# Optimization experiments

Hardware: AMD Instinct MI355X
Metric: run time of the kernel (lower is better)

## Reference

```python
import jax, jax.numpy as jnp
import numpy as np

N = 100000        # nodes
E = 1600000       # edges (avg degree 16)
H = 128           # hidden dim
LAYERS = 3
RESIDUAL = 1.0


def setup_inputs() -> dict:
    key = jax.random.key(0)
    ks = jax.random.split(key, 7)
    x = jax.random.normal(ks[0], (N, H), dtype=jnp.float32)
    src = jax.random.randint(ks[1], (E,), 0, N, dtype=jnp.int32)
    dst = jax.random.randint(ks[2], (E,), 0, N, dtype=jnp.int32)
    s = 1.0 / np.sqrt(H)
    W1 = jax.random.normal(ks[3], (H, H), dtype=jnp.float32) * s
    b1 = jnp.zeros((H,), dtype=jnp.float32)
    W2 = jax.random.normal(ks[4], (H, H), dtype=jnp.float32) * s
    b2 = jnp.zeros((H,), dtype=jnp.float32)
    return {"x": x, "src": src, "dst": dst, "W1": W1, "b1": b1, "W2": W2, "b2": b2}


def _gcn_conv(h, src, dst, dinv, W, b):
    # PyG GCNConv: h' = D^{-1/2}(A+I)D^{-1/2} (h W) + b
    h = h @ W                                   # [N,H]
    norm = dinv[src] * dinv[dst]                # [E]
    msgs = h[src] * norm[:, None]               # [E,H] gather (memory-bound)
    agg = jax.ops.segment_sum(msgs, dst, num_segments=N)  # scatter-add
    agg = agg + h * (dinv * dinv)[:, None]      # self-loop contribution
    return agg + b


def reference(x, src, dst, W1, b1, W2, b2):
    # symmetric degree normalization with self-loops (deg over dst, + 1 for self-loop)
    deg = jax.ops.segment_sum(jnp.ones((E,), x.dtype), dst, num_segments=N) + 1.0
    dinv = jax.lax.rsqrt(deg)                   # [N]

    ori = x
    h = _gcn_conv(x, src, dst, dinv, W1, b1) + RESIDUAL * ori
    for _ in range(LAYERS - 1):
        h = jax.nn.relu(h)                      # dropout is identity in eval mode
        h = _gcn_conv(h, src, dst, dinv, W2, b2) + RESIDUAL * ori
    return h
```

## Files before the change

kernel.cpp:

```cpp
#include <hip/hip_runtime.h>

#define H 128
#define AP 136
#define BSH 9
#define BSZ 512
#define NBK 256

typedef __attribute__((ext_vector_type(8))) short short8;
typedef __attribute__((ext_vector_type(4))) float floatx4;
typedef __attribute__((ext_vector_type(2))) float f32x2;

__device__ inline unsigned short f2b(float f) {
  union { float f; unsigned u; } v; v.f = f;
  unsigned r = v.u + 0x7fffu + ((v.u >> 16) & 1u);
  return (unsigned short)(r >> 16);
}
__device__ inline float blo(unsigned u) { return __uint_as_float(u << 16); }
__device__ inline float bhi(unsigned u) { return __uint_as_float(u & 0xffff0000u); }
__device__ inline unsigned char f2f8(float f) {
  return (unsigned char)(__builtin_amdgcn_cvt_pk_fp8_f32(f, f, 0, false) & 0xff);
}
__device__ inline f32x2 fp8x2(unsigned u) {
#if __has_builtin(__builtin_amdgcn_cvt_pk_f32_fp8)
  return __builtin_amdgcn_cvt_pk_f32_fp8(u, false);
#else
  f32x2 r;
  r.x = __builtin_amdgcn_cvt_f32_fp8(u, 0);
  r.y = __builtin_amdgcn_cvt_f32_fp8(u, 1);
  return r;
#endif
}


__global__ __launch_bounds__(256) void k_bh(const int* __restrict__ dst,
                                            int* __restrict__ bhist,
                                            int E, int NB, int chunk) {
  __shared__ int hst[NBK];
  int tid = threadIdx.x;
  hst[tid] = 0;
  __syncthreads();
  int s = blockIdx.x * chunk;
  int eend = min(s + chunk, E);
  for (int e = s + tid; e < eend; e += 256)
    atomicAdd(&hst[dst[e] >> BSH], 1);
  __syncthreads();
  if (tid < NB) bhist[tid * NBK + blockIdx.x] = hst[tid];
}

__global__ __launch_bounds__(1024) void k_bscan(const int* __restrict__ bhist,
                                                int* __restrict__ boff2,
                                                int total) {
  __shared__ int ps[1024];
  int tid = threadIdx.x;
  int per = (total + 1023) >> 10;
  int s0 = min(tid * per, total), s1 = min(s0 + per, total);
  int sum = 0;
  for (int i = s0; i < s1; i++) sum += bhist[i];
  ps[tid] = sum;
  __syncthreads();
  for (int off = 1; off < 1024; off <<= 1) {
    int t = (tid >= off) ? ps[tid - off] : 0;
    __syncthreads();
    ps[tid] += t;
    __syncthreads();
  }
  int run = ps[tid] - sum;
  for (int i = s0; i < s1; i++) { int v = bhist[i]; boff2[i] = run; run += v; }
}

__global__ __launch_bounds__(256) void k_bscatter(const int* __restrict__ src,
                                                  const int* __restrict__ dst,
                                                  const int* __restrict__ boff2,
                                                  int* __restrict__ bed,
                                                  int E, int NB, int chunk) {
  __shared__ int pos[NBK];
  int tid = threadIdx.x;
  if (tid < NB) pos[tid] = boff2[tid * NBK + blockIdx.x];
  __syncthreads();
  int s = blockIdx.x * chunk;
  int eend = min(s + chunk, E);
  for (int e = s + tid; e < eend; e += 256) {
    int d = dst[e];
    int p = atomicAdd(&pos[d >> BSH], 1);
    bed[p] = (src[e] << BSH) | (d & (BSZ - 1));
  }
}

__global__ __launch_bounds__(512) void k_build(const int* __restrict__ bed,
                                               const int* __restrict__ boff2,
                                               int* __restrict__ roff,
                                               float* __restrict__ dinv,
                                               int* __restrict__ csr,
                                               int N, int E, int NB) {
  __shared__ int cnt[BSZ];
  __shared__ int pos[BSZ];
  __shared__ int ps[BSZ];
  int b = blockIdx.x, tid = threadIdx.x;
  int bs = boff2[b * NBK];
  int be = (b + 1 < NB) ? boff2[(b + 1) * NBK] : E;
  int n0 = b << BSH;
  cnt[tid] = 0;
  __syncthreads();
  for (int e = bs + tid; e < be; e += 512)
    atomicAdd(&cnt[bed[e] & (BSZ - 1)], 1);
  __syncthreads();
  int c = cnt[tid];
  ps[tid] = c;
  __syncthreads();
  for (int off = 1; off < 512; off <<= 1) {
    int t = (tid >= off) ? ps[tid - off] : 0;
    __syncthreads();
    ps[tid] += t;
    __syncthreads();
  }
  int base = bs + ps[tid] - c;
  pos[tid] = base;
  int node = n0 + tid;
  if (node < N) {
    roff[node] = base;
    dinv[node] = rsqrtf((float)c + 1.0f);
  }
  __syncthreads();
  for (int e = bs + tid; e < be; e += 512) {
    int v = bed[e];
    int p = atomicAdd(&pos[v & (BSZ - 1)], 1);
    csr[p] = v >> BSH;
  }
  if (b == 0 && tid == 0) roff[N] = E;
}

__global__ __launch_bounds__(256) void k_prep_w(const float* __restrict__ W1,
                                                const float* __restrict__ W2,
                                                unsigned short* __restrict__ Wt1,
                                                unsigned short* __restrict__ Wt2) {
  const float* W = blockIdx.x ? W2 : W1;
  unsigned short* Wt = blockIdx.x ? Wt2 : Wt1;
  int tid = threadIdx.x;
#pragma unroll
  for (int i = 0; i < 64; i++) {
    int idx = tid + 256 * i;
    int k = idx >> 7, n = idx & 127;
    Wt[n * 128 + k] = f2b(W[idx]);
  }
}

__global__ __launch_bounds__(256) void k_prep_xb(const float* __restrict__ x,
                                                 unsigned int* __restrict__ xb, int total) {
  int i = blockIdx.x * 256 + threadIdx.x;
  if (i < total) {
    float2 v = ((const float2*)x)[i];
    xb[i] = (unsigned)f2b(v.x) | ((unsigned)f2b(v.y) << 16);
  }
}

__global__ __launch_bounds__(256) void k_gemm(const unsigned int* __restrict__ in,
                                              const unsigned short* __restrict__ Wt,
                                              unsigned char* __restrict__ out,
                                              int n) {
  __shared__ short As[64 * AP];
  __shared__ short Bs[128 * AP];
  int tid = threadIdx.x;
  int wave = tid >> 6, lane = tid & 63;
  int quad = lane >> 4, l16 = lane & 15;
  int row0 = blockIdx.x * 64;

  const float4* in4 = (const float4*)in;
#pragma unroll
  for (int i = 0; i < 4; i++) {
    int idx = tid + 256 * i;
    int r = idx >> 4, c = idx & 15;
    int gr = row0 + r;
    float4 v = make_float4(0.f, 0.f, 0.f, 0.f);
    if (gr < n) v = in4[(size_t)gr * 16 + c];
    *(float4*)&As[r * AP + c * 8] = v;
  }
  const float4* Wt4 = (const float4*)Wt;
#pragma unroll
  for (int i = 0; i < 8; i++) {
    int idx = tid + 256 * i;
    int nr = idx >> 4, c = idx & 15;
    *(float4*)&Bs[nr * AP + c * 8] = Wt4[nr * 16 + c];
  }
  __syncthreads();

  floatx4 acc[4][2];
#pragma unroll
  for (int mt = 0; mt < 4; mt++)
#pragma unroll
    for (int nt = 0; nt < 2; nt++) acc[mt][nt] = (floatx4)(0.f);

#pragma unroll
  for (int ks = 0; ks < 4; ks++) {
    short8 a[4], b[2];
#pragma unroll
    for (int mt = 0; mt < 4; mt++)
      a[mt] = *(const short8*)&As[(mt * 16 + l16) * AP + ks * 32 + quad * 8];
#pragma unroll
    for (int nt = 0; nt < 2; nt++)
      b[nt] = *(const short8*)&Bs[(wave * 32 + nt * 16 + l16) * AP + ks * 32 + quad * 8];
#pragma unroll
    for (int mt = 0; mt < 4; mt++)
#pragma unroll
      for (int nt = 0; nt < 2; nt++)
        acc[mt][nt] = __builtin_amdgcn_mfma_f32_16x16x32_bf16(a[mt], b[nt], acc[mt][nt], 0, 0, 0);
  }

#pragma unroll
  for (int mt = 0; mt < 4; mt++) {
#pragma unroll
    for (int nt = 0; nt < 2; nt++) {
#pragma unroll
      for (int r = 0; r < 4; r++) {
        int gr = row0 + mt * 16 + quad * 4 + r;
        if (gr < n)
          out[(size_t)gr * H + wave * 32 + nt * 16 + l16] = f2f8(acc[mt][nt][r]);
      }
    }
  }
}

__global__ __launch_bounds__(256) void k_agg(const unsigned short* __restrict__ h,
                                             const int* __restrict__ csr,
                                             const int* __restrict__ roff,
                                             const float* __restrict__ dinv,
                                             const float* __restrict__ bias,
                                             const unsigned int* __restrict__ xb,
                                             float* __restrict__ out32,
                                             unsigned int* __restrict__ out16,
                                             int n, int write16) {
  int wave = threadIdx.x >> 6;
  int lane = threadIdx.x & 63;
  int node = blockIdx.x * 4 + wave;
  if (node >= n) return;

  float di = dinv[node];
  unsigned su = h[(size_t)node * 64 + lane];
  unsigned xu = xb[(size_t)node * 64 + lane];
  float2 bv = ((const float2*)bias)[lane];
  f32x2 sp = fp8x2(su);
  float acc0 = bv.x + blo(xu) + di * di * sp.x;
  float acc1 = bv.y + bhi(xu) + di * di * sp.y;

  int e0 = roff[node], e1 = roff[node + 1];
  int e = e0;
  for (; e + 16 <= e1; e += 16) {
    int eu = __builtin_amdgcn_readfirstlane(e);
    int idx[16];
#pragma unroll
    for (int k = 0; k < 16; k++) idx[k] = __builtin_amdgcn_readfirstlane(csr[eu + k]);
    unsigned u[16];
#pragma unroll
    for (int k = 0; k < 16; k++) u[k] = (h + ((size_t)idx[k] << 6))[lane];
    float cf[16];
#pragma unroll
    for (int k = 0; k < 16; k++) cf[k] = di * dinv[idx[k]];
#pragma unroll
    for (int k = 0; k < 16; k++) {
      f32x2 p = fp8x2(u[k]);
      acc0 += cf[k] * p.x;
      acc1 += cf[k] * p.y;
    }
  }
  for (; e + 4 <= e1; e += 4) {
    int eu = __builtin_amdgcn_readfirstlane(e);
    int idx[4];
#pragma unroll
    for (int k = 0; k < 4; k++) idx[k] = __builtin_amdgcn_readfirstlane(csr[eu + k]);
    unsigned u[4];
#pragma unroll
    for (int k = 0; k < 4; k++) u[k] = (h + ((size_t)idx[k] << 6))[lane];
    float cf[4];
#pragma unroll
    for (int k = 0; k < 4; k++) cf[k] = di * dinv[idx[k]];
#pragma unroll
    for (int k = 0; k < 4; k++) {
      f32x2 p = fp8x2(u[k]);
      acc0 += cf[k] * p.x;
      acc1 += cf[k] * p.y;
    }
  }
  for (; e < e1; e++) {
    int s = csr[e];
    float cf = di * dinv[s];
    unsigned u = h[(size_t)s * 64 + lane];
    f32x2 p = fp8x2(u);
    acc0 += cf * p.x;
    acc1 += cf * p.y;
  }
  if (write16) {
    out16[(size_t)node * 64 + lane] =
        (unsigned)f2b(fmaxf(acc0, 0.f)) | ((unsigned)f2b(fmaxf(acc1, 0.f)) << 16);
  } else {
    ((float2*)out32)[(size_t)node * 64 + lane] = make_float2(acc0, acc1);
  }
}

extern "C" void kernel_launch(void* const* d_in, const int* in_sizes, int n_in,
                              void* d_out, int out_size, void* d_ws, size_t ws_size,
                              hipStream_t stream) {
  const float* x = (const float*)d_in[0];
  const int* src = (const int*)d_in[1];
  const int* dst = (const int*)d_in[2];
  const float* W1 = (const float*)d_in[3];
  const float* b1 = (const float*)d_in[4];
  const float* W2 = (const float*)d_in[5];
  const float* b2 = (const float*)d_in[6];
  int N = in_sizes[0] / H;
  int E = in_sizes[1];
  float* out = (float*)d_out;

  char* p = (char*)d_ws;
  auto alloc = [&](size_t bytes) {
    char* q = p;
    p += (bytes + 255) & ~(size_t)255;
    return q;
  };
  int* roff = (int*)alloc((size_t)(N + 1) * 4);
  float* dinv = (float*)alloc((size_t)N * 4);
  int* csr = (int*)alloc((size_t)E * 4);
  unsigned int* xb = (unsigned int*)alloc((size_t)N * H * 2);
  unsigned char* htmp = (unsigned char*)alloc((size_t)N * H);
  unsigned int* fbuf = (unsigned int*)alloc((size_t)N * H * 2);
  unsigned short* Wt1 = (unsigned short*)alloc(128 * 128 * 2);
  unsigned short* Wt2 = (unsigned short*)alloc(128 * 128 * 2);
  int* bhist = (int*)alloc((size_t)NBK * NBK * 4);
  int* boff2 = (int*)alloc((size_t)NBK * NBK * 4);
  int* bed = (int*)alloc((size_t)E * 4);

  int NB = (N + BSZ - 1) >> BSH;
  int chunk = (E + NBK - 1) / NBK;

  k_bh<<<NBK, 256, 0, stream>>>(dst, bhist, E, NB, chunk);
  k_bscan<<<1, 1024, 0, stream>>>(bhist, boff2, NB * NBK);
  k_bscatter<<<NBK, 256, 0, stream>>>(src, dst, boff2, bed, E, NB, chunk);
  k_build<<<NB, 512, 0, stream>>>(bed, boff2, roff, dinv, csr, N, E, NB);

  k_prep_w<<<2, 256, 0, stream>>>(W1, W2, Wt1, Wt2);
  k_prep_xb<<<(N * (H / 2) + 255) / 256, 256, 0, stream>>>(x, xb, N * (H / 2));

  int gb = (N + 63) / 64;
  int ab = (N + 3) / 4;

  k_gemm<<<gb, 256, 0, stream>>>(xb, Wt1, htmp, N);
  k_agg<<<ab, 256, 0, stream>>>((const unsigned short*)htmp, csr, roff, dinv, b1, xb,
                                nullptr, fbuf, N, 1);
  k_gemm<<<gb, 256, 0, stream>>>(fbuf, Wt2, htmp, N);
  k_agg<<<ab, 256, 0, stream>>>((const unsigned short*)htmp, csr, roff, dinv, b2, xb,
                                nullptr, fbuf, N, 1);
  k_gemm<<<gb, 256, 0, stream>>>(fbuf, Wt2, htmp, N);
  k_agg<<<ab, 256, 0, stream>>>((const unsigned short*)htmp, csr, roff, dinv, b2, xb,
                                out, nullptr, N, 0);
}
```

Before: 458.6 us.

## Halve bucket-sort partition blocks, vectorize bucket scan, merge prep kernels

Cuts the bucket-sort partition count from 256 to 128 edge chunks and rewrites the offset scan to use one thread per bucket row with int4 loads and stores, replacing the strided 1024-thread scan. It also fuses the weight transpose and x-to-bf16 conversion into one launch, saving a kernel launch. Fewer chunks mean fewer histogram entries to scan, but k_bh and k_bscatter now run with less parallelism and more atomics per block.

```diff
diff --git a/kernel.cpp b/kernel.cpp
--- a/kernel.cpp
+++ b/kernel.cpp
@@ -4,7 +4,8 @@
 #define AP 136
 #define BSH 9
 #define BSZ 512
-#define NBK 256
+#define MAXB 256
+#define NBLK 128
 
 typedef __attribute__((ext_vector_type(8))) short short8;
 typedef __attribute__((ext_vector_type(4))) float floatx4;
@@ -35,7 +36,7 @@
 __global__ __launch_bounds__(256) void k_bh(const int* __restrict__ dst,
                                             int* __restrict__ bhist,
                                             int E, int NB, int chunk) {
-  __shared__ int hst[NBK];
+  __shared__ int hst[MAXB];
   int tid = threadIdx.x;
   hst[tid] = 0;
   __syncthreads();
@@ -44,28 +45,43 @@
   for (int e = s + tid; e < eend; e += 256)
     atomicAdd(&hst[dst[e] >> BSH], 1);
   __syncthreads();
-  if (tid < NB) bhist[tid * NBK + blockIdx.x] = hst[tid];
-}
-
-__global__ __launch_bounds__(1024) void k_bscan(const int* __restrict__ bhist,
-                                                int* __restrict__ boff2,
-                                                int total) {
-  __shared__ int ps[1024];
-  int tid = threadIdx.x;
-  int per = (total + 1023) >> 10;
-  int s0 = min(tid * per, total), s1 = min(s0 + per, total);
+  if (tid < NB) bhist[tid * NBLK + blockIdx.x] = hst[tid];
+}
+
+__global__ __launch_bounds__(256) void k_bscan(const int* __restrict__ bhist,
+                                               int* __restrict__ boff2, int NB) {
+  __shared__ int ps[256];
+  int tid = threadIdx.x;
+  int4 v[NBLK / 4];
   int sum = 0;
-  for (int i = s0; i < s1; i++) sum += bhist[i];
+  if (tid < NB) {
+    const int4* row = (const int4*)(bhist + tid * NBLK);
+#pragma unroll
+    for (int j = 0; j < NBLK / 4; j++) v[j] = row[j];
+#pragma unroll
+    for (int j = 0; j < NBLK / 4; j++) sum += v[j].x + v[j].y + v[j].z + v[j].w;
+  }
   ps[tid] = sum;
   __syncthreads();
-  for (int off = 1; off < 1024; off <<= 1) {
+  for (int off = 1; off < 256; off <<= 1) {
     int t = (tid >= off) ? ps[tid - off] : 0;
     __syncthreads();
     ps[tid] += t;
     __syncthreads();
   }
   int run = ps[tid] - sum;
-  for (int i = s0; i < s1; i++) { int v = bhist[i]; boff2[i] = run; run += v; }
+  if (tid < NB) {
+    int4* orow = (int4*)(boff2 + tid * NBLK);
+#pragma unroll
+    for (int j = 0; j < NBLK / 4; j++) {
+      int4 o;
+      o.x = run; run += v[j].x;
+      o.y = run; run += v[j].y;
+      o.z = run; run += v[j].z;
+      o.w = run; run += v[j].w;
+      orow[j] = o;
+    }
+  }
 }
 
 __global__ __launch_bounds__(256) void k_bscatter(const int* __restrict__ src,
@@ -73,9 +89,9 @@
                                                   const int* __restrict__ boff2,
                                                   int* __restrict__ bed,
                                                   int E, int NB, int chunk) {
-  __shared__ int pos[NBK];
-  int tid = threadIdx.x;
-  if (tid < NB) pos[tid] = boff2[tid * NBK + blockIdx.x];
+  __shared__ int pos[MAXB];
+  int tid = threadIdx.x;
+  if (tid < NB) pos[tid] = boff2[tid * NBLK + blockIdx.x];
   __syncthreads();
   int s = blockIdx.x * chunk;
   int eend = min(s + chunk, E);
@@ -96,8 +112,8 @@
   __shared__ int pos[BSZ];
   __shared__ int ps[BSZ];
   int b = blockIdx.x, tid = threadIdx.x;
-  int bs = boff2[b * NBK];
-  int be = (b + 1 < NB) ? boff2[(b + 1) * NBK] : E;
+  int bs = boff2[b * NBLK];
+  int be = (b + 1 < NB) ? boff2[(b + 1) * NBLK] : E;
   int n0 = b << BSH;
   cnt[tid] = 0;
   __syncthreads();
@@ -129,27 +145,28 @@
   if (b == 0 && tid == 0) roff[N] = E;
 }
 
-__global__ __launch_bounds__(256) void k_prep_w(const float* __restrict__ W1,
-                                                const float* __restrict__ W2,
-                                                unsigned short* __restrict__ Wt1,
-                                                unsigned short* __restrict__ Wt2) {
-  const float* W = blockIdx.x ? W2 : W1;
-  unsigned short* Wt = blockIdx.x ? Wt2 : Wt1;
-  int tid = threadIdx.x;
-#pragma unroll
-  for (int i = 0; i < 64; i++) {
-    int idx = tid + 256 * i;
-    int k = idx >> 7, n = idx & 127;
-    Wt[n * 128 + k] = f2b(W[idx]);
-  }
-}
-
-__global__ __launch_bounds__(256) void k_prep_xb(const float* __restrict__ x,
-                                                 unsigned int* __restrict__ xb, int total) {
-  int i = blockIdx.x * 256 + threadIdx.x;
-  if (i < total) {
-    float2 v = ((const float2*)x)[i];
-    xb[i] = (unsigned)f2b(v.x) | ((unsigned)f2b(v.y) << 16);
+__global__ __launch_bounds__(256) void k_prep(const float* __restrict__ W1,
+                                              const float* __restrict__ W2,
+                                              unsigned short* __restrict__ Wt1,
+                                              unsigned short* __restrict__ Wt2,
+                                              const float* __restrict__ x,
+                                              unsigned int* __restrict__ xb, int total) {
+  int tid = threadIdx.x;
+  if (blockIdx.x < 2) {
+    const float* W = blockIdx.x ? W2 : W1;
+    unsigned short* Wt = blockIdx.x ? Wt2 : Wt1;
+#pragma unroll
+    for (int i = 0; i < 64; i++) {
+      int idx = tid + 256 * i;
+      int k = idx >> 7, n = idx & 127;
+      Wt[n * 128 + k] = f2b(W[idx]);
+    }
+  } else {
+    int i = (blockIdx.x - 2) * 256 + tid;
+    if (i < total) {
+      float2 v = ((const float2*)x)[i];
+      xb[i] = (unsigned)f2b(v.x) | ((unsigned)f2b(v.y) << 16);
+    }
   }
 }
 
@@ -323,20 +340,20 @@
   unsigned int* fbuf = (unsigned int*)alloc((size_t)N * H * 2);
   unsigned short* Wt1 = (unsigned short*)alloc(128 * 128 * 2);
   unsigned short* Wt2 = (unsigned short*)alloc(128 * 128 * 2);
-  int* bhist = (int*)alloc((size_t)NBK * NBK * 4);
-  int* boff2 = (int*)alloc((size_t)NBK * NBK * 4);
+  int* bhist = (int*)alloc((size_t)MAXB * NBLK * 4);
+  int* boff2 = (int*)alloc((size_t)MAXB * NBLK * 4);
   int* bed = (int*)alloc((size_t)E * 4);
 
   int NB = (N + BSZ - 1) >> BSH;
-  int chunk = (E + NBK - 1) / NBK;
-
-  k_bh<<<NBK, 256, 0, stream>>>(dst, bhist, E, NB, chunk);
-  k_bscan<<<1, 1024, 0, stream>>>(bhist, boff2, NB * NBK);
-  k_bscatter<<<NBK, 256, 0, stream>>>(src, dst, boff2, bed, E, NB, chunk);
+  int chunk = (E + NBLK - 1) / NBLK;
+
+  k_bh<<<NBLK, 256, 0, stream>>>(dst, bhist, E, NB, chunk);
+  k_bscan<<<1, 256, 0, stream>>>(bhist, boff2, NB);
+  k_bscatter<<<NBLK, 256, 0, stream>>>(src, dst, boff2, bed, E, NB, chunk);
   k_build<<<NB, 512, 0, stream>>>(bed, boff2, roff, dinv, csr, N, E, NB);
 
-  k_prep_w<<<2, 256, 0, stream>>>(W1, W2, Wt1, Wt2);
-  k_prep_xb<<<(N * (H / 2) + 255) / 256, 256, 0, stream>>>(x, xb, N * (H / 2));
+  int xtotal = N * (H / 2);
+  k_prep<<<2 + (xtotal + 255) / 256, 256, 0, stream>>>(W1, W2, Wt1, Wt2, x, xb, xtotal);
 
   int gb = (N + 63) / 64;
   int ab = (N + 3) / 4;
```

Result: faster. 427.2 us (-6.8%).
